# Optimization experiments

Hardware: AMD Instinct MI355X
Metric: run time of the kernel (lower is better)

Reference implementation:

```python
import jax, jax.numpy as jnp
import numpy as np

D_MODEL, D_K, D_V = 128, 64, 64

def setup_inputs() -> dict:
    key = jax.random.key(0)
    ks = jax.random.split(key, 9)
    B, S = 4, 4096
    q_in = jax.random.normal(ks[0], (B, S, D_MODEL), dtype=jnp.float32)
    k_in = jax.random.normal(ks[1], (B, S, D_MODEL), dtype=jnp.float32)
    v_in = jax.random.normal(ks[2], (B, S, D_MODEL), dtype=jnp.float32)
    # glorot_uniform for kernels; original also uses glorot for biases
    def glorot(k, fan_in, fan_out, shape):
        lim = np.sqrt(6.0 / (fan_in + fan_out))
        return jax.random.uniform(k, shape, jnp.float32, -lim, lim)
    Wq = glorot(ks[3], D_MODEL, D_K, (D_MODEL, D_K)); bq = glorot(ks[4], D_MODEL, D_K, (D_K,))
    Wk = glorot(ks[5], D_MODEL, D_K, (D_MODEL, D_K)); bk = glorot(ks[6], D_MODEL, D_K, (D_K,))
    Wv = glorot(ks[7], D_MODEL, D_V, (D_MODEL, D_V)); bv = glorot(ks[8], D_MODEL, D_V, (D_V,))
    return {"q_in": q_in, "k_in": k_in, "v_in": v_in,
            "Wq": Wq, "bq": bq, "Wk": Wk, "bk": bk, "Wv": Wv, "bv": bv}

def reference(q_in, k_in, v_in, Wq, bq, Wk, bk, Wv, bv):
    q = q_in @ Wq + bq                      # [B,S,d_k]
    k = k_in @ Wk + bk                      # [B,S,d_k]
    v = v_in @ Wv + bv                      # [B,S,d_v]
    scores = jnp.einsum('bqd,bkd->bqk', q, k) / jnp.sqrt(jnp.float32(D_K))
    attn = jax.nn.softmax(scores, axis=-1)  # [B,S,S]
    return jnp.einsum('bqk,bkd->bqd', attn, v)
```

## Files before the change

### kernel.cpp

```cpp
#include <hip/hip_runtime.h>
#include <hip/hip_bf16.h>


using f32x4  = __attribute__((ext_vector_type(4)))  float;
using f32x16 = __attribute__((ext_vector_type(16))) float;
using s16x8  = __attribute__((ext_vector_type(8)))  short;

#define MFMA16(a, b, c) __builtin_amdgcn_mfma_f32_16x16x32_bf16((a), (b), (c), 0, 0, 0)
#define MFMA32(a, b, c) __builtin_amdgcn_mfma_f32_32x32x16_bf16((a), (b), (c), 0, 0, 0)

constexpr int SEQ = 4096;
constexpr int DM  = 128;
constexpr int DV  = 64;
constexpr int B_  = 4;
constexpr float LOG2E = 1.44269504f;
constexpr float SHIFT = 16.0f;

static __device__ __forceinline__ unsigned short f2bf(float f) {
  union { float f; unsigned u; } x; x.f = f;
  unsigned r = x.u + 0x7fffu + ((x.u >> 16) & 1u);
  return (unsigned short)(r >> 16);
}

static __device__ __forceinline__ unsigned cvt_pk_bf16(float lo, float hi) {
  unsigned d;
  asm("v_cvt_pk_bf16_f32 %0, %1, %2" : "=v"(d) : "v"(lo), "v"(hi));
  return d;
}

static __device__ __forceinline__ float bf2f(unsigned short h) {
  union { unsigned u; float f; } x; x.u = ((unsigned)h) << 16;
  return x.f;
}

static __device__ __forceinline__ float exp2_hw(float x) {
  float d;
  asm("v_exp_f32 %0, %1" : "=v"(d) : "v"(x));
  return d;
}

static __device__ __forceinline__ void gll16(const unsigned short* g,
                                             unsigned short* l) {
  __builtin_amdgcn_global_load_lds(
      (const __attribute__((address_space(1))) unsigned int*)g,
      (__attribute__((address_space(3))) unsigned int*)l, 16, 0, 0);
}

__global__ __launch_bounds__(256) void proj_kernel(
    const float* __restrict__ q_in, const float* __restrict__ k_in,
    const float* __restrict__ v_in,
    const float* __restrict__ Wq, const float* __restrict__ bq,
    const float* __restrict__ Wk, const float* __restrict__ bk,
    const float* __restrict__ Wv, const float* __restrict__ bv,
    unsigned short* __restrict__ qp, unsigned short* __restrict__ kp,
    unsigned short* __restrict__ vpT)
{
  __shared__ unsigned short Wt[64][136];
  const int tid = threadIdx.x;
  const int m = blockIdx.y;
  const float* W    = (m == 0) ? Wq : (m == 1) ? Wk : Wv;
  const float* in   = (m == 0) ? q_in : (m == 1) ? k_in : v_in;
  const float* bias = (m == 0) ? bq : (m == 1) ? bk : bv;

  for (int idx = tid; idx < DM * DV; idx += 256) {
    const int k = idx >> 6, c = idx & 63;
    Wt[c][k] = f2bf(W[idx]);
  }
  __syncthreads();

  const int w = tid >> 6, l = tid & 63;
  const int lr = l & 15, lg = l >> 4;
  const int rowbase = blockIdx.x * 64 + w * 16;

  f32x4 acc[4] = {};
  #pragma unroll
  for (int ks = 0; ks < 4; ++ks) {
    const float* ap = in + (size_t)(rowbase + lr) * DM + ks * 32 + lg * 8;
    const float4 a0 = *(const float4*)ap;
    const float4 a1 = *(const float4*)(ap + 4);
    s16x8 af;
    af[0] = (short)f2bf(a0.x); af[1] = (short)f2bf(a0.y);
    af[2] = (short)f2bf(a0.z); af[3] = (short)f2bf(a0.w);
    af[4] = (short)f2bf(a1.x); af[5] = (short)f2bf(a1.y);
    af[6] = (short)f2bf(a1.z); af[7] = (short)f2bf(a1.w);
    #pragma unroll
    for (int nt = 0; nt < 4; ++nt) {
      const s16x8 bfm = *(const s16x8*)&Wt[nt * 16 + lr][ks * 32 + lg * 8];
      acc[nt] = MFMA16(af, bfm, acc[nt]);
    }
  }
  const float scale = (m == 0) ? 0.125f : 1.0f;
  #pragma unroll
  for (int nt = 0; nt < 4; ++nt) {
    const int col = nt * 16 + lr;
    const float bb = bias[col];
    #pragma unroll
    for (int r = 0; r < 4; ++r) {
      const int row = rowbase + lg * 4 + r;
      const unsigned short val = f2bf((acc[nt][r] + bb) * scale);
      if (m == 0)      qp[(size_t)row * DV + col] = val;
      else if (m == 1) kp[(size_t)row * DV + col] = val;
      else             vpT[((size_t)(row >> 12) * DV + col) * SEQ + (row & (SEQ - 1))] = val;
    }
  }
}

static __device__ __forceinline__ s16x8 lds_read_sw(const unsigned short* base,
                                                    int row, int cb) {
  return *(const s16x8*)((const char*)base + row * 128 + (cb ^ ((row & 7) << 4)));
}

__global__ __launch_bounds__(256, 4) void attn_split_kernel(
    const unsigned short* __restrict__ qp, const unsigned short* __restrict__ kp,
    const unsigned short* __restrict__ vpT,
    unsigned short* __restrict__ OpartH, float* __restrict__ lpart,
    float* __restrict__ dout, int klen)
{
  __shared__ unsigned short Kl[2][64 * 64];
  __shared__ unsigned short Vt[2][64 * 64];

  const int tid = threadIdx.x, wq = tid >> 6, l = tid & 63;
  const int l31 = l & 31, hi = l >> 5;
  const int b = blockIdx.y, sp = blockIdx.z;
  const size_t boff = (size_t)b * SEQ * DV;
  const int qrow = blockIdx.x * 128 + wq * 32 + l31;
  const int kstart = sp * klen, kend = kstart + klen;

  s16x8 qf[4];
  {
    const unsigned short* qpr = qp + boff + (size_t)qrow * DV + 8 * hi;
    #pragma unroll
    for (int ks = 0; ks < 4; ++ks)
      qf[ks] = *(const s16x8*)(qpr + 16 * ks);
  }

  const int lrow8 = l >> 3;
  const int xsw   = (((l & 7) ^ (lrow8 & 7)) << 4) >> 1;
  const int c0 = 2 * wq, c1 = 2 * wq + 1;
  const unsigned short* kgb = kp + boff;
  const unsigned short* vgb = vpT + boff;

  #define STAGE_TILE(buf, kb_) do {                                          \
    const unsigned short* kR0 = kgb + (size_t)((kb_) + 8*c0 + lrow8) * DV + xsw; \
    const unsigned short* kR1 = kgb + (size_t)((kb_) + 8*c1 + lrow8) * DV + xsw; \
    gll16(kR0, &Kl[buf][c0 * 512]);                                          \
    gll16(kR1, &Kl[buf][c1 * 512]);                                          \
    const unsigned short* vR0 = vgb + (size_t)(8*c0 + lrow8) * SEQ + (kb_) + xsw; \
    const unsigned short* vR1 = vgb + (size_t)(8*c1 + lrow8) * SEQ + (kb_) + xsw; \
    gll16(vR0, &Vt[buf][c0 * 512]);                                          \
    gll16(vR1, &Vt[buf][c1 * 512]);                                          \
  } while (0)

  STAGE_TILE(0, kstart);
  __syncthreads();

  f32x16 oacc[2] = {};
  f32x4 lacc4 = {};
  int cur = 0;

  for (int kb = kstart; kb < kend; kb += 64) {
    const bool more = (kb + 64 < kend);
    if (more) STAGE_TILE(cur ^ 1, kb + 64);

    const unsigned short* Kc = Kl[cur];
    f32x16 sacc[2] = {};
    __builtin_amdgcn_s_setprio(1);
    #pragma unroll
    for (int ks = 0; ks < 4; ++ks) {
      const int cb = 32 * ks + 16 * hi;
      const s16x8 kf0 = lds_read_sw(Kc, l31, cb);
      const s16x8 kf1 = lds_read_sw(Kc, 32 + l31, cb);
      sacc[0] = MFMA32(kf0, qf[ks], sacc[0]);
      sacc[1] = MFMA32(kf1, qf[ks], sacc[1]);
    }
    __builtin_amdgcn_s_setprio(0);

    #pragma unroll
    for (int mt = 0; mt < 2; ++mt)
      #pragma unroll
      for (int i = 0; i < 16; ++i)
        sacc[mt][i] = exp2_hw(fmaf(sacc[mt][i], LOG2E, -SHIFT));

    {
      float t8[8];
      #pragma unroll
      for (int i = 0; i < 8; ++i)
        t8[i] = (sacc[0][i] + sacc[0][i + 8]) + (sacc[1][i] + sacc[1][i + 8]);
      #pragma unroll
      for (int i = 0; i < 4; ++i) lacc4[i] += t8[i] + t8[i + 4];
    }

    const unsigned short* Vc = Vt[cur];
    __builtin_amdgcn_s_setprio(1);
    #pragma unroll
    for (int ki = 0; ki < 4; ++ki) {
      const int mt = ki >> 1, w8 = (ki & 1) * 8;
      unsigned a0 = cvt_pk_bf16(sacc[mt][w8 + 0], sacc[mt][w8 + 1]);
      unsigned a1 = cvt_pk_bf16(sacc[mt][w8 + 2], sacc[mt][w8 + 3]);
      unsigned b0 = cvt_pk_bf16(sacc[mt][w8 + 4], sacc[mt][w8 + 5]);
      unsigned b1 = cvt_pk_bf16(sacc[mt][w8 + 6], sacc[mt][w8 + 7]);
      asm("v_permlane32_swap_b32 %0, %1" : "+v"(a0), "+v"(b0));
      asm("v_permlane32_swap_b32 %0, %1" : "+v"(a1), "+v"(b1));
      union { unsigned u[4]; s16x8 v; } pf;
      pf.u[0] = a0; pf.u[1] = a1; pf.u[2] = b0; pf.u[3] = b1;
      const int cb = 32 * ki + 16 * hi;
      const s16x8 vf0 = lds_read_sw(Vc, l31, cb);
      const s16x8 vf1 = lds_read_sw(Vc, 32 + l31, cb);
      oacc[0] = MFMA32(vf0, pf.v, oacc[0]);
      oacc[1] = MFMA32(vf1, pf.v, oacc[1]);
    }
    __builtin_amdgcn_s_setprio(0);

    __syncthreads();
    cur ^= 1;
  }
  #undef STAGE_TILE

  float lsum = (lacc4[0] + lacc4[1]) + (lacc4[2] + lacc4[3]);
  lsum += __shfl_xor(lsum, 32);
  const float rinv = 1.0f / lsum;

  if (dout) {
    float* op = dout + boff + (size_t)qrow * DV;
    #pragma unroll
    for (int mt = 0; mt < 2; ++mt)
      #pragma unroll
      for (int g = 0; g < 4; ++g) {
        const int d0 = 32 * mt + 8 * g + 4 * hi;
        float4 v4;
        v4.x = oacc[mt][4 * g + 0] * rinv; v4.y = oacc[mt][4 * g + 1] * rinv;
        v4.z = oacc[mt][4 * g + 2] * rinv; v4.w = oacc[mt][4 * g + 3] * rinv;
        *(float4*)(op + d0) = v4;
      }
  } else {
    const size_t po = ((size_t)sp * B_ + b) * SEQ * DV;
    unsigned short* op = OpartH + po + (size_t)qrow * DV;
    #pragma unroll
    for (int mt = 0; mt < 2; ++mt)
      #pragma unroll
      for (int g = 0; g < 4; ++g) {
        const int d0 = 32 * mt + 8 * g + 4 * hi;
        uint2 u2;
        u2.x = cvt_pk_bf16(oacc[mt][4 * g + 0] * rinv, oacc[mt][4 * g + 1] * rinv);
        u2.y = cvt_pk_bf16(oacc[mt][4 * g + 2] * rinv, oacc[mt][4 * g + 3] * rinv);
        *(uint2*)(op + d0) = u2;
      }
    if (l < 32) {
      const size_t mo = ((size_t)sp * B_ + b) * SEQ + blockIdx.x * 128 + wq * 32 + l;
      lpart[mo] = lsum;
    }
  }
}

__global__ __launch_bounds__(256) void combine_kernel(
    const unsigned short* __restrict__ OpartH, const float* __restrict__ lpart,
    float* __restrict__ out, int nsplit)
{
  const int g = blockIdx.x * 256 + threadIdx.x;
  const int row = g >> 3;
  const int c8 = g & 7;
  const size_t rstride = (size_t)B_ * SEQ;

  float denom = 0.0f;
  float o[8] = {};
  for (int sp = 0; sp < nsplit; ++sp) {
    const float wgt = lpart[sp * rstride + row];
    denom += wgt;
    const s16x8 h = *(const s16x8*)&OpartH[sp * rstride * DV + (size_t)row * DV + c8 * 8];
    #pragma unroll
    for (int j = 0; j < 8; ++j) o[j] += wgt * bf2f((unsigned short)h[j]);
  }
  const float inv = 1.0f / denom;
  float4 v0, v1;
  v0.x = o[0] * inv; v0.y = o[1] * inv; v0.z = o[2] * inv; v0.w = o[3] * inv;
  v1.x = o[4] * inv; v1.y = o[5] * inv; v1.z = o[6] * inv; v1.w = o[7] * inv;
  float* op = out + (size_t)row * DV + c8 * 8;
  *(float4*)op = v0;
  *(float4*)(op + 4) = v1;
}

extern "C" void kernel_launch(void* const* d_in, const int* in_sizes, int n_in,
                              void* d_out, int out_size, void* d_ws, size_t ws_size,
                              hipStream_t stream) {
  const float* q_in = (const float*)d_in[0];
  const float* k_in = (const float*)d_in[1];
  const float* v_in = (const float*)d_in[2];
  const float* Wq   = (const float*)d_in[3];
  const float* bq   = (const float*)d_in[4];
  const float* Wk   = (const float*)d_in[5];
  const float* bk   = (const float*)d_in[6];
  const float* Wv   = (const float*)d_in[7];
  const float* bv   = (const float*)d_in[8];

  const size_t nproj = (size_t)B_ * SEQ * DV;
  unsigned short* qp  = (unsigned short*)d_ws;
  unsigned short* kp  = qp + nproj;
  unsigned short* vpT = kp + nproj;
  char* after = (char*)(vpT + nproj);
  const size_t used_base = (size_t)((char*)after - (char*)d_ws);

  int nsplit = 8;
  while (nsplit > 1) {
    const size_t need = used_base + (size_t)nsplit * B_ * SEQ * (DV * 2 + 4);
    if (need <= ws_size) break;
    nsplit >>= 1;
  }
  const bool direct = (nsplit == 1) &&
      (used_base + (size_t)B_ * SEQ * (DV * 2 + 4) > ws_size);

  unsigned short* OpartH = (unsigned short*)after;
  float* lpart = (float*)(OpartH + (size_t)nsplit * B_ * SEQ * DV);
  float* out = (float*)d_out;

  proj_kernel<<<dim3(256, 3), dim3(256), 0, stream>>>(
      q_in, k_in, v_in, Wq, bq, Wk, bk, Wv, bv, qp, kp, vpT);

  attn_split_kernel<<<dim3(SEQ / 128, B_, nsplit), dim3(256), 0, stream>>>(
      qp, kp, vpT, direct ? nullptr : OpartH, lpart,
      direct ? out : nullptr, SEQ / nsplit);

  if (!direct) {
    combine_kernel<<<dim3(B_ * SEQ * DV / 8 / 256), dim3(256), 0, stream>>>(
        OpartH, lpart, out, nsplit);
  }
}
```

Before: 46.38 us.

## Load V fragments directly from global memory into registers, dropping LDS staging

```diff
diff --git a/kernel.cpp b/kernel.cpp
--- a/kernel.cpp
+++ b/kernel.cpp
@@ -117,7 +117,6 @@
     float* __restrict__ dout, int klen)
 {
   __shared__ unsigned short Kl[2][64 * 64];
-  __shared__ unsigned short Vt[2][64 * 64];
 
   const int tid = threadIdx.x, wq = tid >> 6, l = tid & 63;
   const int l31 = l & 31, hi = l >> 5;
@@ -138,20 +137,16 @@
   const int xsw   = (((l & 7) ^ (lrow8 & 7)) << 4) >> 1;
   const int c0 = 2 * wq, c1 = 2 * wq + 1;
   const unsigned short* kgb = kp + boff;
-  const unsigned short* vgb = vpT + boff;
-
-  #define STAGE_TILE(buf, kb_) do {                                          \
+  const unsigned short* vgb = vpT + boff + (size_t)l31 * SEQ + 8 * hi;
+
+  #define STAGE_K(buf, kb_) do {                                             \
     const unsigned short* kR0 = kgb + (size_t)((kb_) + 8*c0 + lrow8) * DV + xsw; \
     const unsigned short* kR1 = kgb + (size_t)((kb_) + 8*c1 + lrow8) * DV + xsw; \
     gll16(kR0, &Kl[buf][c0 * 512]);                                          \
     gll16(kR1, &Kl[buf][c1 * 512]);                                          \
-    const unsigned short* vR0 = vgb + (size_t)(8*c0 + lrow8) * SEQ + (kb_) + xsw; \
-    const unsigned short* vR1 = vgb + (size_t)(8*c1 + lrow8) * SEQ + (kb_) + xsw; \
-    gll16(vR0, &Vt[buf][c0 * 512]);                                          \
-    gll16(vR1, &Vt[buf][c1 * 512]);                                          \
   } while (0)
 
-  STAGE_TILE(0, kstart);
+  STAGE_K(0, kstart);
   __syncthreads();
 
   f32x16 oacc[2] = {};
@@ -160,7 +155,7 @@
 
   for (int kb = kstart; kb < kend; kb += 64) {
     const bool more = (kb + 64 < kend);
-    if (more) STAGE_TILE(cur ^ 1, kb + 64);
+    if (more) STAGE_K(cur ^ 1, kb + 64);
 
     const unsigned short* Kc = Kl[cur];
     f32x16 sacc[2] = {};
@@ -175,6 +170,14 @@
     }
     __builtin_amdgcn_s_setprio(0);
 
+    const unsigned short* vrow = vgb + kb;
+    s16x8 vfA[4], vfB[4];
+    #pragma unroll
+    for (int ki = 0; ki < 4; ++ki) {
+      vfA[ki] = *(const s16x8*)(vrow + 16 * ki);
+      vfB[ki] = *(const s16x8*)(vrow + 32 * SEQ + 16 * ki);
+    }
+
     #pragma unroll
     for (int mt = 0; mt < 2; ++mt)
       #pragma unroll
@@ -190,7 +193,6 @@
       for (int i = 0; i < 4; ++i) lacc4[i] += t8[i] + t8[i + 4];
     }
 
-    const unsigned short* Vc = Vt[cur];
     __builtin_amdgcn_s_setprio(1);
     #pragma unroll
     for (int ki = 0; ki < 4; ++ki) {
@@ -203,18 +205,15 @@
       asm("v_permlane32_swap_b32 %0, %1" : "+v"(a1), "+v"(b1));
       union { unsigned u[4]; s16x8 v; } pf;
       pf.u[0] = a0; pf.u[1] = a1; pf.u[2] = b0; pf.u[3] = b1;
-      const int cb = 32 * ki + 16 * hi;
-      const s16x8 vf0 = lds_read_sw(Vc, l31, cb);
-      const s16x8 vf1 = lds_read_sw(Vc, 32 + l31, cb);
-      oacc[0] = MFMA32(vf0, pf.v, oacc[0]);
-      oacc[1] = MFMA32(vf1, pf.v, oacc[1]);
+      oacc[0] = MFMA32(vfA[ki], pf.v, oacc[0]);
+      oacc[1] = MFMA32(vfB[ki], pf.v, oacc[1]);
     }
     __builtin_amdgcn_s_setprio(0);
 
     __syncthreads();
     cur ^= 1;
   }
-  #undef STAGE_TILE
+  #undef STAGE_K
 
   float lsum = (lacc4[0] + lacc4[1]) + (lacc4[2] + lacc4[3]);
   lsum += __shfl_xor(lsum, 32);
```

Result: slower. 69.95 us (+50.8%).
